# Performance work log

Measured on AMD Instinct MI355X. Metric: run time of the kernel, lower is better.

Reference implementation:

```python
import jax, jax.numpy as jnp
import numpy as np

N_NODES = 1_000_000
N_EDGES = 5_000_000


def setup_inputs() -> dict:
    key = jax.random.key(0)
    k1, k2, k3, k4 = jax.random.split(key, 4)
    x = jax.random.normal(k1, (N_NODES, 1), dtype=jnp.float32)
    edge_index = jax.random.randint(k2, (2, N_EDGES), 0, N_NODES, dtype=jnp.int64)
    # GCNConv params: lin weight (in,out) applied before propagation, bias after.
    W1 = jax.random.normal(k3, (1, 16), dtype=jnp.float32) / jnp.sqrt(1.0)
    b1 = jnp.zeros((16,), dtype=jnp.float32)
    W2 = jax.random.normal(k4, (16, 1), dtype=jnp.float32) / jnp.sqrt(16.0)
    b2 = jnp.zeros((1,), dtype=jnp.float32)
    return {"x": x, "edge_index": edge_index, "W1": W1, "b1": b1, "W2": W2, "b2": b2}


def _gcn_conv(x, W, b, src, dst, n_nodes):
    """GCNConv: out = D^{-1/2} (A + I) D^{-1/2} (x W) + b."""
    h = x @ W  # [N, F_out]
    loops = jnp.arange(n_nodes, dtype=src.dtype)
    s = jnp.concatenate([src, loops])  # [E+N]
    d = jnp.concatenate([dst, loops])
    # degree from destination index (edge weights = 1), incl. self loops
    deg = jax.ops.segment_sum(jnp.ones_like(d, dtype=h.dtype), d, num_segments=n_nodes)
    dinv = jnp.where(deg > 0, jax.lax.rsqrt(deg), 0.0)
    norm = dinv[s] * dinv[d]  # [E+N]
    msg = h[s] * norm[:, None]  # gather + scale, [E+N, F_out]
    out = jax.ops.segment_sum(msg, d, num_segments=n_nodes)  # scatter-add
    return out + b


def reference(x, edge_index, W1, b1, W2, b2):
    src, dst = edge_index[0], edge_index[1]
    n = x.shape[0]
    h = jax.nn.relu(_gcn_conv(x, W1, b1, src, dst, n))
    return _gcn_conv(h, W2, b2, src, dst, n)
```

## Files before the change

kernel.cpp:

```cpp
#include <hip/hip_runtime.h>

#define THREADS 256
#define BSH 11
#define BSZ 2048
#define NBMAX 512
#define ST 8192
#define SCT 512
#define EPT 16
#define BT 1024


__global__ void k_init(unsigned* __restrict__ gcur, unsigned C, int NB) {
    int t = threadIdx.x;
    if (t < NB) gcur[t] = (unsigned)t * C;
}

__global__ void __launch_bounds__(SCT)
k_scatter(const int* __restrict__ src,
          const int* __restrict__ dst, int E,
          unsigned* __restrict__ gcur,
          unsigned* __restrict__ packed, unsigned C, int NB) {
    __shared__ unsigned tcnt[NBMAX];
    __shared__ unsigned toff[NBMAX];
    __shared__ unsigned gb[NBMAX];
    __shared__ unsigned sh[NBMAX];
    __shared__ unsigned sorted[ST];
    __shared__ unsigned short jarr[ST];

    int tid = threadIdx.x;
    int lo = blockIdx.x * ST;
    int cnt = E - lo; if (cnt > ST) cnt = ST;

    tcnt[tid] = 0u;
    tcnt[tid + SCT < NBMAX ? tid + SCT : tid] = 0u;
    __syncthreads();

    unsigned jreg[EPT], rreg[EPT], rank[EPT];
    #pragma unroll
    for (int kk = 0; kk < EPT / 4; ++kk) {
        int g = kk * SCT + tid;
        int base = g * 4;
        if (base + 3 < cnt) {
            int4 d4 = *(const int4*)(dst + lo + base);
            int4 s4 = *(const int4*)(src + lo + base);
            unsigned j0 = (unsigned)d4.x >> BSH;
            unsigned j1 = (unsigned)d4.y >> BSH;
            unsigned j2 = (unsigned)d4.z >> BSH;
            unsigned j3 = (unsigned)d4.w >> BSH;
            jreg[kk*4+0] = j0; rreg[kk*4+0] = (unsigned)s4.x | (((unsigned)d4.x & (BSZ-1)) << 20);
            jreg[kk*4+1] = j1; rreg[kk*4+1] = (unsigned)s4.y | (((unsigned)d4.y & (BSZ-1)) << 20);
            jreg[kk*4+2] = j2; rreg[kk*4+2] = (unsigned)s4.z | (((unsigned)d4.z & (BSZ-1)) << 20);
            jreg[kk*4+3] = j3; rreg[kk*4+3] = (unsigned)s4.w | (((unsigned)d4.w & (BSZ-1)) << 20);
            rank[kk*4+0] = atomicAdd(&tcnt[j0], 1u);
            rank[kk*4+1] = atomicAdd(&tcnt[j1], 1u);
            rank[kk*4+2] = atomicAdd(&tcnt[j2], 1u);
            rank[kk*4+3] = atomicAdd(&tcnt[j3], 1u);
        } else {
            #pragma unroll
            for (int c = 0; c < 4; ++c) {
                int idx = base + c;
                if (idx < cnt) {
                    int d = dst[lo + idx];
                    unsigned jj = (unsigned)d >> BSH;
                    jreg[kk*4+c] = jj;
                    rreg[kk*4+c] = (unsigned)src[lo + idx] | (((unsigned)d & (BSZ-1)) << 20);
                    rank[kk*4+c] = atomicAdd(&tcnt[jj], 1u);
                } else {
                    jreg[kk*4+c] = ~0u;
                }
            }
        }
    }
    __syncthreads();

    unsigned v = tcnt[tid];
    sh[tid] = v;
    __syncthreads();
    for (int off = 1; off < NBMAX; off <<= 1) {
        unsigned t = (tid >= off) ? sh[tid - off] : 0u;
        __syncthreads();
        sh[tid] += t;
        __syncthreads();
    }
    {
        unsigned excl = sh[tid] - v;
        toff[tid] = excl;
        if (v) gb[tid] = atomicAdd(&gcur[tid], v);
    }
    __syncthreads();

    #pragma unroll
    for (int k = 0; k < EPT; ++k) {
        unsigned jj = jreg[k];
        if (jj != ~0u) {
            unsigned p = toff[jj] + rank[k];
            sorted[p] = rreg[k];
            jarr[p] = (unsigned short)jj;
        }
    }
    __syncthreads();

    for (int p = tid; p < cnt; p += SCT) {
        unsigned jj = jarr[p];
        unsigned pos = gb[jj] + ((unsigned)p - toff[jj]);
        if (pos < (jj + 1u) * C) packed[pos] = sorted[p];
    }
}

__global__ void k_deg(const unsigned* __restrict__ packed,
                      const unsigned* __restrict__ gcur, unsigned C,
                      const float* __restrict__ x,
                      float* __restrict__ dinv, float* __restrict__ y, int N) {
    int j = blockIdx.x;
    __shared__ unsigned cntl[BSZ];
    for (int t = threadIdx.x; t < BSZ; t += BT) cntl[t] = 0u;
    __syncthreads();
    unsigned e0 = (unsigned)j * C;
    unsigned e1 = gcur[j]; if (e1 > e0 + C) e1 = e0 + C;
    unsigned tid = threadIdx.x;
    unsigned nv4 = (e1 - e0) >> 2;
    unsigned g = tid;
    for (; g + BT < nv4; g += 2u * BT) {
        uint4 a = *(const uint4*)(packed + e0 + (size_t)g * 4u);
        uint4 b = *(const uint4*)(packed + e0 + (size_t)(g + BT) * 4u);
        atomicAdd(&cntl[a.x >> 20], 1u);
        atomicAdd(&cntl[a.y >> 20], 1u);
        atomicAdd(&cntl[a.z >> 20], 1u);
        atomicAdd(&cntl[a.w >> 20], 1u);
        atomicAdd(&cntl[b.x >> 20], 1u);
        atomicAdd(&cntl[b.y >> 20], 1u);
        atomicAdd(&cntl[b.z >> 20], 1u);
        atomicAdd(&cntl[b.w >> 20], 1u);
    }
    for (; g < nv4; g += BT) {
        uint4 a = *(const uint4*)(packed + e0 + (size_t)g * 4u);
        atomicAdd(&cntl[a.x >> 20], 1u);
        atomicAdd(&cntl[a.y >> 20], 1u);
        atomicAdd(&cntl[a.z >> 20], 1u);
        atomicAdd(&cntl[a.w >> 20], 1u);
    }
    for (unsigned e = e0 + nv4 * 4u + tid; e < e1; e += BT)
        atomicAdd(&cntl[packed[e] >> 20], 1u);
    __syncthreads();
    int base = j << BSH;
    for (int t = threadIdx.x; t < BSZ; t += BT) {
        int v = base + t;
        if (v < N) {
            float d = rsqrtf((float)cntl[t] + 1.0f);
            dinv[v] = d;
            y[v] = x[v] * d;
        }
    }
}

__global__ void k_acc1(const unsigned* __restrict__ packed,
                       const unsigned* __restrict__ gcur, unsigned C,
                       const float* __restrict__ y,
                       const float* __restrict__ dinv,
                       const float* __restrict__ W1,
                       const float* __restrict__ b1,
                       const float* __restrict__ W2,
                       float* __restrict__ zy, int N, int F) {
    int j = blockIdx.x;
    __shared__ float acc[BSZ];
    __shared__ float w1s[64], b1s[64], w2s[64];
    for (int t = threadIdx.x; t < BSZ; t += BT) acc[t] = 0.f;
    if (threadIdx.x < (unsigned)F) {
        w1s[threadIdx.x] = W1[threadIdx.x];
        b1s[threadIdx.x] = b1[threadIdx.x];
        w2s[threadIdx.x] = W2[threadIdx.x];
    }
    __syncthreads();
    unsigned e0 = (unsigned)j * C;
    unsigned e1 = gcur[j]; if (e1 > e0 + C) e1 = e0 + C;
    unsigned tid = threadIdx.x;
    unsigned nv4 = (e1 - e0) >> 2;
    unsigned g = tid;
    for (; g + BT < nv4; g += 2u * BT) {
        uint4 a = *(const uint4*)(packed + e0 + (size_t)g * 4u);
        uint4 b = *(const uint4*)(packed + e0 + (size_t)(g + BT) * 4u);
        float v0 = y[a.x & 0xFFFFFu], v1 = y[a.y & 0xFFFFFu];
        float v2 = y[a.z & 0xFFFFFu], v3 = y[a.w & 0xFFFFFu];
        float v4 = y[b.x & 0xFFFFFu], v5 = y[b.y & 0xFFFFFu];
        float v6 = y[b.z & 0xFFFFFu], v7 = y[b.w & 0xFFFFFu];
        atomicAdd(&acc[a.x >> 20], v0);
        atomicAdd(&acc[a.y >> 20], v1);
        atomicAdd(&acc[a.z >> 20], v2);
        atomicAdd(&acc[a.w >> 20], v3);
        atomicAdd(&acc[b.x >> 20], v4);
        atomicAdd(&acc[b.y >> 20], v5);
        atomicAdd(&acc[b.z >> 20], v6);
        atomicAdd(&acc[b.w >> 20], v7);
    }
    for (; g < nv4; g += BT) {
        uint4 a = *(const uint4*)(packed + e0 + (size_t)g * 4u);
        float v0 = y[a.x & 0xFFFFFu], v1 = y[a.y & 0xFFFFFu];
        float v2 = y[a.z & 0xFFFFFu], v3 = y[a.w & 0xFFFFFu];
        atomicAdd(&acc[a.x >> 20], v0);
        atomicAdd(&acc[a.y >> 20], v1);
        atomicAdd(&acc[a.z >> 20], v2);
        atomicAdd(&acc[a.w >> 20], v3);
    }
    for (unsigned e = e0 + nv4 * 4u + tid; e < e1; e += BT) {
        unsigned p = packed[e];
        atomicAdd(&acc[p >> 20], y[p & 0xFFFFFu]);
    }
    __syncthreads();
    int base = j << BSH;
    for (int t = threadIdx.x; t < BSZ; t += BT) {
        int v = base + t;
        if (v < N) {
            float d = dinv[v];
            float agg = d * (acc[t] + y[v]);
            float z = 0.f;
            for (int f = 0; f < F; ++f) {
                float h = fmaf(w1s[f], agg, b1s[f]);
                h = fmaxf(h, 0.f);
                z = fmaf(h, w2s[f], z);
            }
            zy[v] = z * d;
        }
    }
}

__global__ void k_out(const unsigned* __restrict__ packed,
                      const unsigned* __restrict__ gcur, unsigned C,
                      const float* __restrict__ zy,
                      const float* __restrict__ dinv,
                      const float* __restrict__ b2,
                      float* __restrict__ out, int N) {
    int j = blockIdx.x;
    __shared__ float acc[BSZ];
    for (int t = threadIdx.x; t < BSZ; t += BT) acc[t] = 0.f;
    __syncthreads();
    unsigned e0 = (unsigned)j * C;
    unsigned e1 = gcur[j]; if (e1 > e0 + C) e1 = e0 + C;
    unsigned tid = threadIdx.x;
    unsigned nv4 = (e1 - e0) >> 2;
    unsigned g = tid;
    for (; g + BT < nv4; g += 2u * BT) {
        uint4 a = *(const uint4*)(packed + e0 + (size_t)g * 4u);
        uint4 b = *(const uint4*)(packed + e0 + (size_t)(g + BT) * 4u);
        float v0 = zy[a.x & 0xFFFFFu], v1 = zy[a.y & 0xFFFFFu];
        float v2 = zy[a.z & 0xFFFFFu], v3 = zy[a.w & 0xFFFFFu];
        float v4 = zy[b.x & 0xFFFFFu], v5 = zy[b.y & 0xFFFFFu];
        float v6 = zy[b.z & 0xFFFFFu], v7 = zy[b.w & 0xFFFFFu];
        atomicAdd(&acc[a.x >> 20], v0);
        atomicAdd(&acc[a.y >> 20], v1);
        atomicAdd(&acc[a.z >> 20], v2);
        atomicAdd(&acc[a.w >> 20], v3);
        atomicAdd(&acc[b.x >> 20], v4);
        atomicAdd(&acc[b.y >> 20], v5);
        atomicAdd(&acc[b.z >> 20], v6);
        atomicAdd(&acc[b.w >> 20], v7);
    }
    for (; g < nv4; g += BT) {
        uint4 a = *(const uint4*)(packed + e0 + (size_t)g * 4u);
        float v0 = zy[a.x & 0xFFFFFu], v1 = zy[a.y & 0xFFFFFu];
        float v2 = zy[a.z & 0xFFFFFu], v3 = zy[a.w & 0xFFFFFu];
        atomicAdd(&acc[a.x >> 20], v0);
        atomicAdd(&acc[a.y >> 20], v1);
        atomicAdd(&acc[a.z >> 20], v2);
        atomicAdd(&acc[a.w >> 20], v3);
    }
    for (unsigned e = e0 + nv4 * 4u + tid; e < e1; e += BT) {
        unsigned p = packed[e];
        atomicAdd(&acc[p >> 20], zy[p & 0xFFFFFu]);
    }
    __syncthreads();
    int base = j << BSH;
    for (int t = threadIdx.x; t < BSZ; t += BT) {
        int v = base + t;
        if (v < N)
            out[v] = fmaf(dinv[v], acc[t] + zy[v], b2[0]);
    }
}


__global__ void f_zero3(float* __restrict__ a, float* __restrict__ b,
                        float* __restrict__ c, int N) {
    int i = blockIdx.x * blockDim.x + threadIdx.x;
    int stride = gridDim.x * blockDim.x;
    for (int v = i; v < N; v += stride) { a[v] = 0.f; b[v] = 0.f; c[v] = 0.f; }
}
__global__ void f_deg(const int* __restrict__ dst, int E, float* __restrict__ degf) {
    int i = blockIdx.x * blockDim.x + threadIdx.x;
    int stride = gridDim.x * blockDim.x;
    for (int e = i; e < E; e += stride) atomicAdd(&degf[dst[e]], 1.0f);
}
__global__ void f_dinv(float* __restrict__ d, int N) {
    int v = blockIdx.x * blockDim.x + threadIdx.x;
    if (v < N) d[v] = rsqrtf(d[v] + 1.0f);
}
__global__ void f_edge1(const int* __restrict__ src, const int* __restrict__ dst,
                        const float* __restrict__ x, const float* __restrict__ dinv,
                        float* __restrict__ acc1, int E) {
    int i = blockIdx.x * blockDim.x + threadIdx.x;
    int stride = gridDim.x * blockDim.x;
    for (int e = i; e < E; e += stride) {
        int s = src[e];
        atomicAdd(&acc1[dst[e]], x[s] * dinv[s]);
    }
}
__global__ void f_node2(const float* __restrict__ dinv, const float* __restrict__ acc1,
                        const float* __restrict__ x, const float* __restrict__ W1,
                        const float* __restrict__ b1, const float* __restrict__ W2,
                        float* __restrict__ zy, int N, int F) {
    int v = blockIdx.x * blockDim.x + threadIdx.x;
    if (v < N) {
        float d = dinv[v];
        float agg = d * (acc1[v] + x[v] * d);
        float z = 0.f;
        for (int f = 0; f < F; ++f) {
            float h = fmaf(W1[f], agg, b1[f]);
            h = h > 0.f ? h : 0.f;
            z = fmaf(h, W2[f], z);
        }
        zy[v] = z * d;
    }
}
__global__ void f_edge2(const int* __restrict__ src, const int* __restrict__ dst,
                        const float* __restrict__ zy, float* __restrict__ out, int E) {
    int i = blockIdx.x * blockDim.x + threadIdx.x;
    int stride = gridDim.x * blockDim.x;
    for (int e = i; e < E; e += stride) atomicAdd(&out[dst[e]], zy[src[e]]);
}
__global__ void f_node3(const float* __restrict__ dinv, const float* __restrict__ zy,
                        const float* __restrict__ b2, float* __restrict__ out, int N) {
    int v = blockIdx.x * blockDim.x + threadIdx.x;
    if (v < N) out[v] = fmaf(dinv[v], out[v] + zy[v], b2[0]);
}


extern "C" void kernel_launch(void* const* d_in, const int* in_sizes, int n_in,
                              void* d_out, int out_size, void* d_ws, size_t ws_size,
                              hipStream_t stream) {
    const float* x  = (const float*)d_in[0];
    const int*   ei = (const int*)d_in[1];
    const float* W1 = (const float*)d_in[2];
    const float* b1 = (const float*)d_in[3];
    const float* W2 = (const float*)d_in[4];
    const float* b2 = (const float*)d_in[5];
    float* out = (float*)d_out;

    const int N = in_sizes[0];
    const int E = in_sizes[1] / 2;
    const int F = in_sizes[2];

    const int* src = ei;
    const int* dst = ei + E;

    const int NB = (N + BSZ - 1) >> BSH;

    unsigned mean = (unsigned)(E / (NB > 0 ? NB : 1));
    unsigned C = (mean + mean / 8u + 1024u + 3u) & ~3u;

    size_t off_packed = 0;
    size_t off_gc     = (off_packed + (size_t)NB * C * 4 + 15) & ~(size_t)15;
    size_t off_dinv   = (off_gc + (size_t)NBMAX * 4 + 15) & ~(size_t)15;
    size_t off_y      = off_dinv + (size_t)N * 4;
    size_t off_zy     = off_y + (size_t)N * 4;
    size_t need       = off_zy + (size_t)N * 4;

    bool ok = (ws_size >= need) && (NB >= 1) && (NB <= NBMAX) &&
              (N <= (1 << 20)) && (F <= 64) && (E > 0);

    char* ws = (char*)d_ws;
    if (ok) {
        unsigned* packed = (unsigned*)(ws + off_packed);
        unsigned* gcur   = (unsigned*)(ws + off_gc);
        float*    dinv   = (float*)(ws + off_dinv);
        float*    y      = (float*)(ws + off_y);
        float*    zy     = (float*)(ws + off_zy);

        int scatBlocks = (E + ST - 1) / ST;

        k_init   <<<1, NBMAX, 0, stream>>>(gcur, C, NB);
        k_scatter<<<scatBlocks, SCT, 0, stream>>>(src, dst, E, gcur, packed, C, NB);
        k_deg    <<<NB, BT, 0, stream>>>(packed, gcur, C, x, dinv, y, N);
        k_acc1   <<<NB, BT, 0, stream>>>(packed, gcur, C, y, dinv, W1, b1, W2, zy, N, F);
        k_out    <<<NB, BT, 0, stream>>>(packed, gcur, C, zy, dinv, b2, out, N);
    } else {
        float* dinv = (float*)(ws);
        float* acc1 = (float*)(ws + (size_t)N * 4);
        float* zy   = (float*)(ws + (size_t)N * 8);
        int nodeBlocks = (N + THREADS - 1) / THREADS;
        int edgeBlocks = (E + THREADS - 1) / THREADS;
        if (edgeBlocks > 2048) edgeBlocks = 2048;
        f_zero3<<<2048, THREADS, 0, stream>>>(dinv, acc1, out, N);
        f_deg  <<<edgeBlocks, THREADS, 0, stream>>>(dst, E, dinv);
        f_dinv <<<nodeBlocks, THREADS, 0, stream>>>(dinv, N);
        f_edge1<<<edgeBlocks, THREADS, 0, stream>>>(src, dst, x, dinv, acc1, E);
        f_node2<<<nodeBlocks, THREADS, 0, stream>>>(dinv, acc1, x, W1, b1, W2, zy, N, F);
        f_edge2<<<edgeBlocks, THREADS, 0, stream>>>(src, dst, zy, out, E);
        f_node3<<<nodeBlocks, THREADS, 0, stream>>>(dinv, zy, b2, out, N);
    }
}
```

Measured before the change: 109.3 us.

## Fuse degree and two aggregation passes into one cooperative kernel with LDS-cached edges

Replaces the three per-bucket kernels (degree, first aggregation, output) with a single cooperative kernel that separates the phases with grid-wide syncs. Each block loads its bucket's packed edge records into LDS once and reuses them across all three phases, so the packed array is not reread from global memory and two kernel launches go away. In exchange the kernel needs about 67KB of LDS per 1024-thread block, requires every bucket block to be co-resident, and adds grid-sync cost; if the occupancy check fails it falls back to the old kernels. It also simplifies the fallback kernels' unrolled loops and removes one redundant tcnt zeroing in the scatter kernel.

```diff
diff --git a/kernel.cpp b/kernel.cpp
--- a/kernel.cpp
+++ b/kernel.cpp
@@ -1,4 +1,7 @@
 #include <hip/hip_runtime.h>
+#include <hip/hip_cooperative_groups.h>
+
+namespace cg = cooperative_groups;
 
 #define THREADS 256
 #define BSH 11
@@ -8,6 +11,8 @@
 #define SCT 512
 #define EPT 16
 #define BT 1024
+#define LDSE 12800
+#define SMASK 0xFFFFFu
 
 
 __global__ void k_init(unsigned* __restrict__ gcur, unsigned C, int NB) {
@@ -32,7 +37,6 @@
     int cnt = E - lo; if (cnt > ST) cnt = ST;
 
     tcnt[tid] = 0u;
-    tcnt[tid + SCT < NBMAX ? tid + SCT : tid] = 0u;
     __syncthreads();
 
     unsigned jreg[EPT], rreg[EPT], rank[EPT];
@@ -107,6 +111,124 @@
     }
 }
 
+__global__ void __launch_bounds__(BT, 8)
+k_fused(const unsigned* __restrict__ packed,
+        const unsigned* __restrict__ gcur, unsigned C,
+        const float* __restrict__ x,
+        const float* __restrict__ W1, const float* __restrict__ b1,
+        const float* __restrict__ W2, const float* __restrict__ b2,
+        float* __restrict__ dinv, float* __restrict__ y,
+        float* __restrict__ zy, float* __restrict__ out,
+        int N, int F) {
+    cg::grid_group grid = cg::this_grid();
+    __shared__ __align__(16) unsigned recs[LDSE];
+    __shared__ unsigned cntl[BSZ];
+    __shared__ float    accf[BSZ];
+    __shared__ float    w1s[64], b1s[64], w2s[64];
+
+    const int j = blockIdx.x;
+    const unsigned tid = threadIdx.x;
+    const int base = j << BSH;
+
+    for (int t = tid; t < BSZ; t += BT) cntl[t] = 0u;
+    if (tid < (unsigned)F) {
+        w1s[tid] = W1[tid]; b1s[tid] = b1[tid]; w2s[tid] = W2[tid];
+    }
+    __syncthreads();
+
+    unsigned e0 = (unsigned)j * C;
+    unsigned e1 = gcur[j]; if (e1 > e0 + C) e1 = e0 + C;
+    const unsigned n = e1 - e0;
+    const unsigned nv4 = n >> 2;
+
+    for (unsigned g = tid; g < nv4; g += BT) {
+        uint4 a = *(const uint4*)(packed + e0 + (size_t)g * 4u);
+        ((uint4*)recs)[g] = a;
+        atomicAdd(&cntl[a.x >> 20], 1u);
+        atomicAdd(&cntl[a.y >> 20], 1u);
+        atomicAdd(&cntl[a.z >> 20], 1u);
+        atomicAdd(&cntl[a.w >> 20], 1u);
+    }
+    for (unsigned e = nv4 * 4u + tid; e < n; e += BT) {
+        unsigned p = packed[e0 + e];
+        recs[e] = p;
+        atomicAdd(&cntl[p >> 20], 1u);
+    }
+    __syncthreads();
+    for (int t = tid; t < BSZ; t += BT) {
+        int v = base + t;
+        if (v < N) {
+            float d = rsqrtf((float)cntl[t] + 1.0f);
+            dinv[v] = d;
+            y[v] = x[v] * d;
+        }
+    }
+    grid.sync();
+
+    for (int t = tid; t < BSZ; t += BT) accf[t] = 0.f;
+    __syncthreads();
+    {
+        unsigned i = tid;
+        for (; i + 3u * BT < n; i += 4u * BT) {
+            unsigned p0 = recs[i],          p1 = recs[i + BT];
+            unsigned p2 = recs[i + 2u*BT],  p3 = recs[i + 3u*BT];
+            float v0 = y[p0 & SMASK], v1 = y[p1 & SMASK];
+            float v2 = y[p2 & SMASK], v3 = y[p3 & SMASK];
+            atomicAdd(&accf[p0 >> 20], v0);
+            atomicAdd(&accf[p1 >> 20], v1);
+            atomicAdd(&accf[p2 >> 20], v2);
+            atomicAdd(&accf[p3 >> 20], v3);
+        }
+        for (; i < n; i += BT) {
+            unsigned p = recs[i];
+            atomicAdd(&accf[p >> 20], y[p & SMASK]);
+        }
+    }
+    __syncthreads();
+    for (int t = tid; t < BSZ; t += BT) {
+        int v = base + t;
+        if (v < N) {
+            float d = dinv[v];
+            float agg = d * (accf[t] + y[v]);
+            float z = 0.f;
+            for (int f = 0; f < F; ++f) {
+                float h = fmaf(w1s[f], agg, b1s[f]);
+                h = fmaxf(h, 0.f);
+                z = fmaf(h, w2s[f], z);
+            }
+            zy[v] = z * d;
+        }
+    }
+    grid.sync();
+
+    for (int t = tid; t < BSZ; t += BT) accf[t] = 0.f;
+    __syncthreads();
+    {
+        unsigned i = tid;
+        for (; i + 3u * BT < n; i += 4u * BT) {
+            unsigned p0 = recs[i],          p1 = recs[i + BT];
+            unsigned p2 = recs[i + 2u*BT],  p3 = recs[i + 3u*BT];
+            float v0 = zy[p0 & SMASK], v1 = zy[p1 & SMASK];
+            float v2 = zy[p2 & SMASK], v3 = zy[p3 & SMASK];
+            atomicAdd(&accf[p0 >> 20], v0);
+            atomicAdd(&accf[p1 >> 20], v1);
+            atomicAdd(&accf[p2 >> 20], v2);
+            atomicAdd(&accf[p3 >> 20], v3);
+        }
+        for (; i < n; i += BT) {
+            unsigned p = recs[i];
+            atomicAdd(&accf[p >> 20], zy[p & SMASK]);
+        }
+    }
+    __syncthreads();
+    for (int t = tid; t < BSZ; t += BT) {
+        int v = base + t;
+        if (v < N)
+            out[v] = fmaf(dinv[v], accf[t] + zy[v], b2[0]);
+    }
+}
+
+
 __global__ void k_deg(const unsigned* __restrict__ packed,
                       const unsigned* __restrict__ gcur, unsigned C,
                       const float* __restrict__ x,
@@ -119,20 +241,7 @@
     unsigned e1 = gcur[j]; if (e1 > e0 + C) e1 = e0 + C;
     unsigned tid = threadIdx.x;
     unsigned nv4 = (e1 - e0) >> 2;
-    unsigned g = tid;
-    for (; g + BT < nv4; g += 2u * BT) {
-        uint4 a = *(const uint4*)(packed + e0 + (size_t)g * 4u);
-        uint4 b = *(const uint4*)(packed + e0 + (size_t)(g + BT) * 4u);
-        atomicAdd(&cntl[a.x >> 20], 1u);
-        atomicAdd(&cntl[a.y >> 20], 1u);
-        atomicAdd(&cntl[a.z >> 20], 1u);
-        atomicAdd(&cntl[a.w >> 20], 1u);
-        atomicAdd(&cntl[b.x >> 20], 1u);
-        atomicAdd(&cntl[b.y >> 20], 1u);
-        atomicAdd(&cntl[b.z >> 20], 1u);
-        atomicAdd(&cntl[b.w >> 20], 1u);
-    }
-    for (; g < nv4; g += BT) {
+    for (unsigned g = tid; g < nv4; g += BT) {
         uint4 a = *(const uint4*)(packed + e0 + (size_t)g * 4u);
         atomicAdd(&cntl[a.x >> 20], 1u);
         atomicAdd(&cntl[a.y >> 20], 1u);
@@ -175,35 +284,18 @@
     unsigned e1 = gcur[j]; if (e1 > e0 + C) e1 = e0 + C;
     unsigned tid = threadIdx.x;
     unsigned nv4 = (e1 - e0) >> 2;
-    unsigned g = tid;
-    for (; g + BT < nv4; g += 2u * BT) {
+    for (unsigned g = tid; g < nv4; g += BT) {
         uint4 a = *(const uint4*)(packed + e0 + (size_t)g * 4u);
-        uint4 b = *(const uint4*)(packed + e0 + (size_t)(g + BT) * 4u);
-        float v0 = y[a.x & 0xFFFFFu], v1 = y[a.y & 0xFFFFFu];
-        float v2 = y[a.z & 0xFFFFFu], v3 = y[a.w & 0xFFFFFu];
-        float v4 = y[b.x & 0xFFFFFu], v5 = y[b.y & 0xFFFFFu];
-        float v6 = y[b.z & 0xFFFFFu], v7 = y[b.w & 0xFFFFFu];
+        float v0 = y[a.x & SMASK], v1 = y[a.y & SMASK];
+        float v2 = y[a.z & SMASK], v3 = y[a.w & SMASK];
         atomicAdd(&acc[a.x >> 20], v0);
         atomicAdd(&acc[a.y >> 20], v1);
         atomicAdd(&acc[a.z >> 20], v2);
         atomicAdd(&acc[a.w >> 20], v3);
-        atomicAdd(&acc[b.x >> 20], v4);
-        atomicAdd(&acc[b.y >> 20], v5);
-        atomicAdd(&acc[b.z >> 20], v6);
-        atomicAdd(&acc[b.w >> 20], v7);
-    }
-    for (; g < nv4; g += BT) {
-        uint4 a = *(const uint4*)(packed + e0 + (size_t)g * 4u);
-        float v0 = y[a.x & 0xFFFFFu], v1 = y[a.y & 0xFFFFFu];
-        float v2 = y[a.z & 0xFFFFFu], v3 = y[a.w & 0xFFFFFu];
-        atomicAdd(&acc[a.x >> 20], v0);
-        atomicAdd(&acc[a.y >> 20], v1);
-        atomicAdd(&acc[a.z >> 20], v2);
-        atomicAdd(&acc[a.w >> 20], v3);
     }
     for (unsigned e = e0 + nv4 * 4u + tid; e < e1; e += BT) {
         unsigned p = packed[e];
-        atomicAdd(&acc[p >> 20], y[p & 0xFFFFFu]);
+        atomicAdd(&acc[p >> 20], y[p & SMASK]);
     }
     __syncthreads();
     int base = j << BSH;
@@ -237,35 +329,18 @@
     unsigned e1 = gcur[j]; if (e1 > e0 + C) e1 = e0 + C;
     unsigned tid = threadIdx.x;
     unsigned nv4 = (e1 - e0) >> 2;
-    unsigned g = tid;
-    for (; g + BT < nv4; g += 2u * BT) {
+    for (unsigned g = tid; g < nv4; g += BT) {
         uint4 a = *(const uint4*)(packed + e0 + (size_t)g * 4u);
-        uint4 b = *(const uint4*)(packed + e0 + (size_t)(g + BT) * 4u);
-        float v0 = zy[a.x & 0xFFFFFu], v1 = zy[a.y & 0xFFFFFu];
-        float v2 = zy[a.z & 0xFFFFFu], v3 = zy[a.w & 0xFFFFFu];
-        float v4 = zy[b.x & 0xFFFFFu], v5 = zy[b.y & 0xFFFFFu];
-        float v6 = zy[b.z & 0xFFFFFu], v7 = zy[b.w & 0xFFFFFu];
+        float v0 = zy[a.x & SMASK], v1 = zy[a.y & SMASK];
+        float v2 = zy[a.z & SMASK], v3 = zy[a.w & SMASK];
         atomicAdd(&acc[a.x >> 20], v0);
         atomicAdd(&acc[a.y >> 20], v1);
         atomicAdd(&acc[a.z >> 20], v2);
         atomicAdd(&acc[a.w >> 20], v3);
-        atomicAdd(&acc[b.x >> 20], v4);
-        atomicAdd(&acc[b.y >> 20], v5);
-        atomicAdd(&acc[b.z >> 20], v6);
-        atomicAdd(&acc[b.w >> 20], v7);
-    }
-    for (; g < nv4; g += BT) {
-        uint4 a = *(const uint4*)(packed + e0 + (size_t)g * 4u);
-        float v0 = zy[a.x & 0xFFFFFu], v1 = zy[a.y & 0xFFFFFu];
-        float v2 = zy[a.z & 0xFFFFFu], v3 = zy[a.w & 0xFFFFFu];
-        atomicAdd(&acc[a.x >> 20], v0);
-        atomicAdd(&acc[a.y >> 20], v1);
-        atomicAdd(&acc[a.z >> 20], v2);
-        atomicAdd(&acc[a.w >> 20], v3);
     }
     for (unsigned e = e0 + nv4 * 4u + tid; e < e1; e += BT) {
         unsigned p = packed[e];
-        atomicAdd(&acc[p >> 20], zy[p & 0xFFFFFu]);
+        atomicAdd(&acc[p >> 20], zy[p & SMASK]);
     }
     __syncthreads();
     int base = j << BSH;
@@ -377,9 +452,33 @@
 
         k_init   <<<1, NBMAX, 0, stream>>>(gcur, C, NB);
         k_scatter<<<scatBlocks, SCT, 0, stream>>>(src, dst, E, gcur, packed, C, NB);
-        k_deg    <<<NB, BT, 0, stream>>>(packed, gcur, C, x, dinv, y, N);
-        k_acc1   <<<NB, BT, 0, stream>>>(packed, gcur, C, y, dinv, W1, b1, W2, zy, N, F);
-        k_out    <<<NB, BT, 0, stream>>>(packed, gcur, C, zy, dinv, b2, out, N);
+
+        bool coop = (C <= LDSE);
+        int occ = 0, cus = 0;
+        if (coop) {
+            if (hipOccupancyMaxActiveBlocksPerMultiprocessor(&occ, k_fused, BT, 0)
+                    != hipSuccess) coop = false;
+            int dev = 0;
+            hipGetDevice(&dev);
+            if (hipDeviceGetAttribute(&cus, hipDeviceAttributeMultiprocessorCount,
+                                      dev) != hipSuccess) coop = false;
+            if (coop && (long long)occ * cus < NB) coop = false;
+        }
+        if (coop) {
+            unsigned Cv = C; int Nv = N, Fv = F;
+            void* args[] = { (void*)&packed, (void*)&gcur, (void*)&Cv,
+                             (void*)&x, (void*)&W1, (void*)&b1, (void*)&W2,
+                             (void*)&b2, (void*)&dinv, (void*)&y, (void*)&zy,
+                             (void*)&out, (void*)&Nv, (void*)&Fv };
+            if (hipLaunchCooperativeKernel((const void*)k_fused, dim3(NB),
+                                           dim3(BT), args, 0, stream)
+                    != hipSuccess) coop = false;
+        }
+        if (!coop) {
+            k_deg  <<<NB, BT, 0, stream>>>(packed, gcur, C, x, dinv, y, N);
+            k_acc1 <<<NB, BT, 0, stream>>>(packed, gcur, C, y, dinv, W1, b1, W2, zy, N, F);
+            k_out  <<<NB, BT, 0, stream>>>(packed, gcur, C, zy, dinv, b2, out, N);
+        }
     } else {
         float* dinv = (float*)(ws);
         float* acc1 = (float*)(ws + (size_t)N * 4);
```

Result: no change. 108.1 us (-1.1%).
